# Kernel tuning notes

Measured on AMD Instinct MI355X. Metric: run time of the kernel, lower is better.

## Reference

```python
import jax, jax.numpy as jnp
import numpy as np

NS = 0.4      # neighborhood_size
GS = 8        # grid_size
RNN = 128     # rnn_size
EMB = 64      # embedding_size
NMIX = 20     # nmixtures
N = 1024      # num pedestrians


def setup_inputs() -> dict:
    key = jax.random.key(0)
    ks = jax.random.split(key, 14)
    s = 0.05
    return {
        "xoff": jax.random.normal(ks[0], (N, 2)) * s,
        "xabs": jax.random.uniform(ks[1], (N, 2)),
        "h0": jax.random.normal(ks[2], (1, N, RNN)) * 0.1,
        "c0": jax.random.normal(ks[3], (1, N, RNN)) * 0.1,
        "W_emb": jax.random.normal(ks[4], (EMB, 2)) * s,
        "b_emb": jax.random.normal(ks[5], (EMB,)) * s,
        "W_soc": jax.random.normal(ks[6], (EMB, GS * GS * RNN)) * s,
        "b_soc": jax.random.normal(ks[7], (EMB,)) * s,
        "W_ih": jax.random.normal(ks[8], (4 * RNN, 2 * EMB)) * s,
        "W_hh": jax.random.normal(ks[9], (4 * RNN, RNN)) * s,
        "b_ih": jax.random.normal(ks[10], (4 * RNN,)) * s,
        "b_hh": jax.random.normal(ks[11], (4 * RNN,)) * s,
        "W_out": jax.random.normal(ks[12], (6 * NMIX, RNN)) * s,
        "b_out": jax.random.normal(ks[13], (6 * NMIX,)) * s,
    }


def grid_mask(xabs, dtype):
    # Vectorized getGridMask: [N, N, GS*GS] one-hot neighbor binning.
    x, y = xabs[:, 0], xabs[:, 1]
    dx = x[None, :] - (x[:, None] - NS / 2)  # other_x - width_low, [N, N]
    dy = y[None, :] - (y[:, None] - NS / 2)
    cx = jnp.floor(dx / NS * GS).astype(jnp.int32)
    cy = jnp.floor(dy / NS * GS).astype(jnp.int32)
    n = x.shape[0]
    valid = ((dx >= 0) & (dx < NS) & (dy >= 0) & (dy < NS)
             & (cx >= 0) & (cx < GS) & (cy >= 0) & (cy < GS)
             & ~jnp.eye(n, dtype=bool))
    cell = jnp.clip(cx + cy * GS, 0, GS * GS - 1)
    return jax.nn.one_hot(cell, GS * GS, dtype=dtype) * valid[..., None].astype(dtype)


def reference(xoff, xabs, h0, c0, W_emb, b_emb, W_soc, b_soc,
              W_ih, W_hh, b_ih, b_hh, W_out, b_out):
    n = xabs.shape[0]
    # predict_distance=True -> embed offsets
    emb = jax.nn.relu(xoff @ W_emb.T + b_emb)                 # [N, 64]
    grid = grid_mask(xabs, emb.dtype)                          # [N, N, 64]
    h = h0[0]                                                  # [N, 128]
    # getSocialTensor: scatter neighbor hidden states into grid bins
    social = jnp.einsum('nmg,mh->ngh', grid, h).reshape(n, GS * GS * RNN)
    pool = jax.nn.relu(social @ W_soc.T + b_soc)               # [N, 64]
    xin = jnp.concatenate([emb, pool], axis=-1)                # [N, 128]
    # single-step LSTM, torch gate order i, f, g, o
    gates = xin @ W_ih.T + h @ W_hh.T + b_ih + b_hh            # [N, 512]
    i, f, g, o = jnp.split(gates, 4, axis=-1)
    c = jax.nn.sigmoid(f) * c0[0] + jax.nn.sigmoid(i) * jnp.tanh(g)
    hn = jax.nn.sigmoid(o) * jnp.tanh(c)
    out = hn @ W_out.T + b_out                                 # [N, 120]
    mu1, mu2, ls1, ls2, rho, pi_logits = jnp.split(out, 6, axis=1)
    return (mu1, mu2, ls1, ls2, rho, pi_logits)
```

## Files before the change

kernel.cpp:

```cpp
#include <hip/hip_runtime.h>
#include <hip/hip_bf16.h>

#define NN_ 1024

#define U_WGF  0
#define U_WOUT 131072
#define U_SHI  147456
#define U_SLO  671744
#define U_ACTH 1196032
#define U_ACTL 1458176
#define U_P    1720320
#define F_GL   2957312

typedef __attribute__((ext_vector_type(8))) short short8;
typedef __attribute__((ext_vector_type(4))) float floatx4;

__device__ __forceinline__ float b2f_(unsigned short u) {
    return __uint_as_float(((unsigned)u) << 16);
}
__device__ __forceinline__ unsigned short f2bu(float f) {
    __hip_bfloat16 b = __float2bfloat16(f);
    return *(unsigned short*)&b;
}
__device__ __forceinline__ float ldin(const void* p, int i, int isbf) {
    return isbf ? b2f_(((const unsigned short*)p)[i]) : ((const float*)p)[i];
}
__device__ __forceinline__ int detect_bf16(const void* Wih, int tid) {
    unsigned wv = ((const unsigned*)Wih)[tid];
    unsigned e8 = (wv >> 7) & 0xFFu;
    return (__syncthreads_count((e8 >= 96u && e8 <= 134u) ? 1 : 0) > 128) ? 1 : 0;
}

__global__ __launch_bounds__(256) void prep_kernel(
        const void* __restrict__ xoff, const void* __restrict__ h0,
        const void* __restrict__ Wsoc, const void* __restrict__ Wemb,
        const void* __restrict__ bemb, const void* __restrict__ Wih,
        const void* __restrict__ Whh,  const void* __restrict__ Wout,
        float* __restrict__ ws) {
    const int tid = threadIdx.x;
    const int isbf = detect_bf16(Wih, tid);
    unsigned short* u = (unsigned short*)ws;
    const int t0 = (blockIdx.x * 256 + tid) * 8;
    unsigned short hv[8], lv[8];
    if (t0 < 131072) {
        int jl = (t0 >> 3) & 15, q = (t0 >> 7) & 3, kb = (t0 >> 9) & 7, jt = t0 >> 12;
        int j = jt * 16 + jl, k0 = kb * 32 + q * 8;
#pragma unroll
        for (int r = 0; r < 8; r++) {
            int k = k0 + r;
            float v = (k < 128) ? ldin(Wih, j * 128 + k, isbf)
                                : ldin(Whh, j * 128 + (k - 128), isbf);
            hv[r] = f2bu(v);
        }
        *(short8*)(u + U_WGF + t0) = *(short8*)hv;
    } else if (t0 < 147456) {
        int t2 = t0 - 131072; int r = t2 >> 7, j0 = t2 & 127;
#pragma unroll
        for (int i = 0; i < 8; i++) {
            int j = j0 + i;
            hv[i] = f2bu((j < 120) ? ldin(Wout, j * 128 + r, isbf) : 0.0f);
        }
        *(short8*)(u + U_WOUT + t2) = *(short8*)hv;
    } else if (t0 < 671744) {
        int t2 = t0 - 147456;
        int e = (t2 >> 3) & 63, q = (t2 >> 9) & 3, j = (t2 >> 11) & 3, g = t2 >> 13;
        int src = e * 8192 + g * 128 + j * 32 + q * 8;
#pragma unroll
        for (int r = 0; r < 8; r++) {
            float x = ldin(Wsoc, src + r, isbf);
            hv[r] = f2bu(x);
            lv[r] = f2bu(x - b2f_(hv[r]));
        }
        *(short8*)(u + U_SHI + t2) = *(short8*)hv;
        *(short8*)(u + U_SLO + t2) = *(short8*)lv;
    } else if (t0 < 802816) {
        int t2 = t0 - 671744; int n = t2 >> 7, k = t2 & 127;
#pragma unroll
        for (int i = 0; i < 8; i++) {
            float x = ldin(h0, t2 + i, isbf);
            hv[i] = f2bu(x);
            lv[i] = f2bu(x - b2f_(hv[i]));
        }
        *(short8*)(u + U_ACTH + n * 256 + 128 + k) = *(short8*)hv;
        *(short8*)(u + U_ACTL + n * 256 + 128 + k) = *(short8*)lv;
    } else {
        int t2 = t0 - 802816; int n = t2 >> 6, e0 = t2 & 63;
        float x0 = ldin(xoff, 2 * n, isbf), x1 = ldin(xoff, 2 * n + 1, isbf);
#pragma unroll
        for (int i = 0; i < 8; i++) {
            int e = e0 + i;
            float v = fmaf(x0, ldin(Wemb, 2 * e, isbf),
                      fmaf(x1, ldin(Wemb, 2 * e + 1, isbf), ldin(bemb, e, isbf)));
            v = fmaxf(v, 0.0f);
            hv[i] = f2bu(v);
            lv[i] = f2bu(v - b2f_(hv[i]));
        }
        *(short8*)(u + U_ACTH + n * 256 + e0) = *(short8*)hv;
        *(short8*)(u + U_ACTL + n * 256 + e0) = *(short8*)lv;
    }
}

__global__ __launch_bounds__(256) void pgemm_kernel(float* __restrict__ ws) {
    const unsigned short* u = (const unsigned short*)ws;
    const short* Ah  = (const short*)(u + U_ACTH);
    const short* Al  = (const short*)(u + U_ACTL);
    const short* Shi = (const short*)(u + U_SHI);
    const short* Slo = (const short*)(u + U_SLO);
    unsigned short* P16 = (unsigned short*)ws + U_P;
    const int tid = threadIdx.x, lane = tid & 63, wv = tid >> 6;
    const int B_ = blockIdx.y * 64 + blockIdx.x;
    const int mtile = B_ & 63, rest = B_ >> 6;
    const int cg = rest >> 1, thalf = rest & 1;
    const int m = lane & 15, q = lane >> 4;
    const int g = cg * 4 + wv;
    const int abase = (mtile * 16 + m) * 256 + 128 + q * 8;
    short8 ah[4], al[4];
#pragma unroll
    for (int j = 0; j < 4; j++) {
        ah[j] = *(const short8*)(Ah + abase + 32 * j);
        al[j] = *(const short8*)(Al + abase + 32 * j);
    }
    const int rowl = mtile * 16 + q * 4;
#pragma unroll
    for (int tt = 0; tt < 2; tt++) {
        const int t = thalf * 2 + tt;
        const int e = t * 16 + m;
        short8 bh[4], bl[4];
#pragma unroll
        for (int j = 0; j < 4; j++) {
            const int fb = ((g * 4 + j) * 4 + q) * 512 + e * 8;
            bh[j] = *(const short8*)(Shi + fb);
            bl[j] = *(const short8*)(Slo + fb);
        }
        floatx4 c = {0.0f, 0.0f, 0.0f, 0.0f};
#pragma unroll
        for (int j = 0; j < 4; j++) c = __builtin_amdgcn_mfma_f32_16x16x32_bf16(ah[j], bh[j], c, 0, 0, 0);
#pragma unroll
        for (int j = 0; j < 4; j++) c = __builtin_amdgcn_mfma_f32_16x16x32_bf16(ah[j], bl[j], c, 0, 0, 0);
#pragma unroll
        for (int j = 0; j < 4; j++) c = __builtin_amdgcn_mfma_f32_16x16x32_bf16(al[j], bh[j], c, 0, 0, 0);
        const int n0 = cg * 256 + wv * 64 + t * 16;
#pragma unroll
        for (int r = 0; r < 4; r++)
            P16[(rowl + r) * 4096 + n0 + m] = f2bu(c[r]);
    }
}

__global__ __launch_bounds__(256) void pool_kernel(const void* __restrict__ xabs,
                                                   const void* __restrict__ b_soc,
                                                   const void* __restrict__ Wih_det,
                                                   float* __restrict__ ws) {
    __shared__ float xabs_s[2048];
    __shared__ int   off[NN_];
    __shared__ int   cnt_s;
    __shared__ float4 red4[16][16];
    const int tid = threadIdx.x;
    const int isbf = detect_bf16(Wih_det, tid);
    const int n = blockIdx.x;
    unsigned short* u = (unsigned short*)ws;

    for (int i = tid; i < 2048; i += 256) xabs_s[i] = ldin(xabs, i, isbf);
    if (tid == 0) cnt_s = 0;
    __syncthreads();
    {
        float xs = xabs_s[2 * n]     - 0.2f;
        float ys = xabs_s[2 * n + 1] - 0.2f;
        for (int i = tid; i < NN_; i += 256) {
            float dx = xabs_s[2 * i]     - xs;
            float dy = xabs_s[2 * i + 1] - ys;
            int cx = (int)floorf(dx / 0.4f * 8.0f);
            int cy = (int)floorf(dy / 0.4f * 8.0f);
            bool valid = (dx >= 0.0f) && (dx < 0.4f) && (dy >= 0.0f) && (dy < 0.4f)
                      && (cx >= 0) && (cx < 8) && (cy >= 0) && (cy < 8) && (i != n);
            if (valid) {
                int idx = atomicAdd(&cnt_s, 1);
                off[idx] = i * 4096 + ((cy * 8 + cx) << 6);
            }
        }
    }
    __syncthreads();
    {
        const unsigned short* P16 = (const unsigned short*)ws + U_P;
        const int strm = tid >> 4, e4 = tid & 15;
        const int cc = cnt_s;
        float ax = 0.0f, ay = 0.0f, az = 0.0f, aw = 0.0f;
        for (int j = strm; j < cc; j += 16) {
            int o = off[j];
            ushort4 uu = *(const ushort4*)(P16 + o + 4 * e4);
            ax += b2f_(uu.x); ay += b2f_(uu.y); az += b2f_(uu.z); aw += b2f_(uu.w);
        }
        red4[strm][e4] = make_float4(ax, ay, az, aw);
    }
    __syncthreads();
    if (tid < 16) {
        float s[4] = {0.0f, 0.0f, 0.0f, 0.0f};
#pragma unroll
        for (int s16 = 0; s16 < 16; s16++) {
            float4 r = red4[s16][tid];
            s[0] += r.x; s[1] += r.y; s[2] += r.z; s[3] += r.w;
        }
        int e = 4 * tid;
#pragma unroll
        for (int i = 0; i < 4; i++) {
            float v = fmaxf(s[i] + ldin(b_soc, e + i, isbf), 0.0f);
            unsigned short hi = f2bu(v);
            u[U_ACTH + n * 256 + 64 + e + i] = hi;
            u[U_ACTL + n * 256 + 64 + e + i] = f2bu(v - b2f_(hi));
        }
    }
}

__global__ __launch_bounds__(256) void gates_kernel(const void* __restrict__ b_ih,
                                                    const void* __restrict__ b_hh,
                                                    const void* __restrict__ Wih_det,
                                                    float* __restrict__ ws) {
    const int tid = threadIdx.x;
    const int isbf = detect_bf16(Wih_det, tid);
    const unsigned short* u = (const unsigned short*)ws;
    const short* Ah = (const short*)(u + U_ACTH);
    const short* Al = (const short*)(u + U_ACTL);
    const short* Wg = (const short*)(u + U_WGF);
    float* gl = ws + F_GL;
    const int lane = tid & 63, wv = tid >> 6, m = lane & 15, q = lane >> 4;
    const int m0 = blockIdx.x * 16;
    const int jt = blockIdx.y * 4 + wv;
    floatx4 acc = {0.0f, 0.0f, 0.0f, 0.0f};
#pragma unroll
    for (int kb = 0; kb < 8; kb++) {
        const int ab = (m0 + m) * 256 + kb * 32 + q * 8;
        short8 ah = *(const short8*)(Ah + ab);
        short8 al = *(const short8*)(Al + ab);
        short8 b  = *(const short8*)(Wg + (jt * 8 + kb) * 512 + q * 128 + m * 8);
        acc = __builtin_amdgcn_mfma_f32_16x16x32_bf16(ah, b, acc, 0, 0, 0);
        acc = __builtin_amdgcn_mfma_f32_16x16x32_bf16(al, b, acc, 0, 0, 0);
    }
    const int j = jt * 16 + m;
    const float bias = ldin(b_ih, j, isbf) + ldin(b_hh, j, isbf);
#pragma unroll
    for (int r = 0; r < 4; r++)
        gl[(m0 + q * 4 + r) * 512 + j] = acc[r] + bias;
}

__global__ __launch_bounds__(256) void pwout_kernel(const void* __restrict__ c0,
                                                    const void* __restrict__ b_out,
                                                    const void* __restrict__ Wih_det,
                                                    const float* __restrict__ ws,
                                                    float* __restrict__ out) {
    __shared__ __align__(16) float hnl[2][128];
    const int tid = threadIdx.x;
    const int isbf = detect_bf16(Wih_det, tid);
    const int n0 = blockIdx.x * 2;
    const unsigned short* u = (const unsigned short*)ws;
    const float* gl = ws + F_GL;
    const int half = tid >> 7, t2 = tid & 127;
    const int n = n0 + half;
    {
        int r = t2;
        float iv = gl[n * 512 + r],       fv = gl[n * 512 + r + 128];
        float gv = gl[n * 512 + r + 256], ov = gl[n * 512 + r + 384];
        float si = 1.0f / (1.0f + expf(-iv));
        float sf = 1.0f / (1.0f + expf(-fv));
        float so = 1.0f / (1.0f + expf(-ov));
        float cc = sf * ldin(c0, n * 128 + r, isbf) + si * tanhf(gv);
        hnl[half][r] = so * tanhf(cc);
    }
    __syncthreads();
    {
        int j = t2;
        if (j < 120) {
            float acc = ldin(b_out, j, isbf);
            for (int r = 0; r < 128; r += 4) {
                float4 hq = *(const float4*)&hnl[half][r];
                acc = fmaf(hq.x, b2f_(u[U_WOUT + (r + 0) * 128 + j]), acc);
                acc = fmaf(hq.y, b2f_(u[U_WOUT + (r + 1) * 128 + j]), acc);
                acc = fmaf(hq.z, b2f_(u[U_WOUT + (r + 2) * 128 + j]), acc);
                acc = fmaf(hq.w, b2f_(u[U_WOUT + (r + 3) * 128 + j]), acc);
            }
            int ch = j / 20, wc = j - ch * 20;
            out[ch * 20480 + n * 20 + wc] = acc;
        }
    }
}

extern "C" void kernel_launch(void* const* d_in, const int* in_sizes, int n_in,
                              void* d_out, int out_size, void* d_ws, size_t ws_size,
                              hipStream_t stream) {
    const void* xoff  = d_in[0];
    const void* xabs  = d_in[1];
    const void* h0    = d_in[2];
    const void* c0    = d_in[3];
    const void* W_emb = d_in[4];
    const void* b_emb = d_in[5];
    const void* W_soc = d_in[6];
    const void* b_soc = d_in[7];
    const void* W_ih  = d_in[8];
    const void* W_hh  = d_in[9];
    const void* b_ih  = d_in[10];
    const void* b_hh  = d_in[11];
    const void* W_out = d_in[12];
    const void* b_out = d_in[13];
    float* ws = (float*)d_ws;
    float* out = (float*)d_out;

    prep_kernel<<<424, 256, 0, stream>>>(xoff, h0, W_soc, W_emb, b_emb,
                                         W_ih, W_hh, W_out, ws);
    pgemm_kernel<<<dim3(64, 32), 256, 0, stream>>>(ws);
    pool_kernel<<<1024, 256, 0, stream>>>(xabs, b_soc, W_ih, ws);
    gates_kernel<<<dim3(64, 8), 256, 0, stream>>>(b_ih, b_hh, W_ih, ws);
    pwout_kernel<<<512, 256, 0, stream>>>(c0, b_out, W_ih, ws, out);
}
```

Measured before the change: 124.6 us.

## Drop split-bf16 compensation, fuse LSTM cell into gates kernel, fp32 Wout

Removes the hi/lo bf16 split of activations and W_soc, so the social GEMM and gate GEMM use one bf16 MFMA pass instead of three or two. This halves the operand traffic and cuts MFMA work. The gate output columns are permuted so each block holds i/f/g/o for the same 16 hidden units, which lets the LSTM cell nonlinearity run inside the gates kernel and write hn directly instead of a 512-wide gate buffer. W_out is now stored in fp32. The cost is lower precision in the pooled and gate results, which could affect accuracy tolerance.

```diff
diff --git a/kernel.cpp b/kernel.cpp
--- a/kernel.cpp
+++ b/kernel.cpp
@@ -4,13 +4,11 @@
 #define NN_ 1024
 
 #define U_WGF  0
-#define U_WOUT 131072
-#define U_SHI  147456
-#define U_SLO  671744
-#define U_ACTH 1196032
-#define U_ACTL 1458176
-#define U_P    1720320
-#define F_GL   2957312
+#define U_SHI  131072
+#define U_ACTH 655360
+#define U_P    917504
+#define F_WOUT 2555904
+#define F_HN   2572288
 
 typedef __attribute__((ext_vector_type(8))) short short8;
 typedef __attribute__((ext_vector_type(4))) float floatx4;
@@ -41,10 +39,11 @@
     const int isbf = detect_bf16(Wih, tid);
     unsigned short* u = (unsigned short*)ws;
     const int t0 = (blockIdx.x * 256 + tid) * 8;
-    unsigned short hv[8], lv[8];
+    unsigned short hv[8];
     if (t0 < 131072) {
         int jl = (t0 >> 3) & 15, q = (t0 >> 7) & 3, kb = (t0 >> 9) & 7, jt = t0 >> 12;
-        int j = jt * 16 + jl, k0 = kb * 32 + q * 8;
+        int j = (jt & 3) * 128 + (jt >> 2) * 16 + jl;
+        int k0 = kb * 32 + q * 8;
 #pragma unroll
         for (int r = 0; r < 8; r++) {
             int k = k0 + r;
@@ -58,31 +57,20 @@
 #pragma unroll
         for (int i = 0; i < 8; i++) {
             int j = j0 + i;
-            hv[i] = f2bu((j < 120) ? ldin(Wout, j * 128 + r, isbf) : 0.0f);
-        }
-        *(short8*)(u + U_WOUT + t2) = *(short8*)hv;
+            ws[F_WOUT + t2 + i] = (j < 120) ? ldin(Wout, j * 128 + r, isbf) : 0.0f;
+        }
     } else if (t0 < 671744) {
         int t2 = t0 - 147456;
         int e = (t2 >> 3) & 63, q = (t2 >> 9) & 3, j = (t2 >> 11) & 3, g = t2 >> 13;
         int src = e * 8192 + g * 128 + j * 32 + q * 8;
 #pragma unroll
-        for (int r = 0; r < 8; r++) {
-            float x = ldin(Wsoc, src + r, isbf);
-            hv[r] = f2bu(x);
-            lv[r] = f2bu(x - b2f_(hv[r]));
-        }
+        for (int r = 0; r < 8; r++) hv[r] = f2bu(ldin(Wsoc, src + r, isbf));
         *(short8*)(u + U_SHI + t2) = *(short8*)hv;
-        *(short8*)(u + U_SLO + t2) = *(short8*)lv;
     } else if (t0 < 802816) {
         int t2 = t0 - 671744; int n = t2 >> 7, k = t2 & 127;
 #pragma unroll
-        for (int i = 0; i < 8; i++) {
-            float x = ldin(h0, t2 + i, isbf);
-            hv[i] = f2bu(x);
-            lv[i] = f2bu(x - b2f_(hv[i]));
-        }
+        for (int i = 0; i < 8; i++) hv[i] = f2bu(ldin(h0, t2 + i, isbf));
         *(short8*)(u + U_ACTH + n * 256 + 128 + k) = *(short8*)hv;
-        *(short8*)(u + U_ACTL + n * 256 + 128 + k) = *(short8*)lv;
     } else {
         int t2 = t0 - 802816; int n = t2 >> 6, e0 = t2 & 63;
         float x0 = ldin(xoff, 2 * n, isbf), x1 = ldin(xoff, 2 * n + 1, isbf);
@@ -91,21 +79,16 @@
             int e = e0 + i;
             float v = fmaf(x0, ldin(Wemb, 2 * e, isbf),
                       fmaf(x1, ldin(Wemb, 2 * e + 1, isbf), ldin(bemb, e, isbf)));
-            v = fmaxf(v, 0.0f);
-            hv[i] = f2bu(v);
-            lv[i] = f2bu(v - b2f_(hv[i]));
+            hv[i] = f2bu(fmaxf(v, 0.0f));
         }
         *(short8*)(u + U_ACTH + n * 256 + e0) = *(short8*)hv;
-        *(short8*)(u + U_ACTL + n * 256 + e0) = *(short8*)lv;
     }
 }
 
 __global__ __launch_bounds__(256) void pgemm_kernel(float* __restrict__ ws) {
     const unsigned short* u = (const unsigned short*)ws;
     const short* Ah  = (const short*)(u + U_ACTH);
-    const short* Al  = (const short*)(u + U_ACTL);
     const short* Shi = (const short*)(u + U_SHI);
-    const short* Slo = (const short*)(u + U_SLO);
     unsigned short* P16 = (unsigned short*)ws + U_P;
     const int tid = threadIdx.x, lane = tid & 63, wv = tid >> 6;
     const int B_ = blockIdx.y * 64 + blockIdx.x;
@@ -114,31 +97,20 @@
     const int m = lane & 15, q = lane >> 4;
     const int g = cg * 4 + wv;
     const int abase = (mtile * 16 + m) * 256 + 128 + q * 8;
-    short8 ah[4], al[4];
-#pragma unroll
-    for (int j = 0; j < 4; j++) {
-        ah[j] = *(const short8*)(Ah + abase + 32 * j);
-        al[j] = *(const short8*)(Al + abase + 32 * j);
-    }
+    short8 ah[4];
+#pragma unroll
+    for (int j = 0; j < 4; j++) ah[j] = *(const short8*)(Ah + abase + 32 * j);
     const int rowl = mtile * 16 + q * 4;
 #pragma unroll
     for (int tt = 0; tt < 2; tt++) {
         const int t = thalf * 2 + tt;
         const int e = t * 16 + m;
-        short8 bh[4], bl[4];
+        floatx4 c = {0.0f, 0.0f, 0.0f, 0.0f};
 #pragma unroll
         for (int j = 0; j < 4; j++) {
-            const int fb = ((g * 4 + j) * 4 + q) * 512 + e * 8;
-            bh[j] = *(const short8*)(Shi + fb);
-            bl[j] = *(const short8*)(Slo + fb);
-        }
-        floatx4 c = {0.0f, 0.0f, 0.0f, 0.0f};
-#pragma unroll
-        for (int j = 0; j < 4; j++) c = __builtin_amdgcn_mfma_f32_16x16x32_bf16(ah[j], bh[j], c, 0, 0, 0);
-#pragma unroll
-        for (int j = 0; j < 4; j++) c = __builtin_amdgcn_mfma_f32_16x16x32_bf16(ah[j], bl[j], c, 0, 0, 0);
-#pragma unroll
-        for (int j = 0; j < 4; j++) c = __builtin_amdgcn_mfma_f32_16x16x32_bf16(al[j], bh[j], c, 0, 0, 0);
+            short8 bh = *(const short8*)(Shi + ((g * 4 + j) * 4 + q) * 512 + e * 8);
+            c = __builtin_amdgcn_mfma_f32_16x16x32_bf16(ah[j], bh, c, 0, 0, 0);
+        }
         const int n0 = cg * 256 + wv * 64 + t * 16;
 #pragma unroll
         for (int r = 0; r < 4; r++)
@@ -203,46 +175,52 @@
 #pragma unroll
         for (int i = 0; i < 4; i++) {
             float v = fmaxf(s[i] + ldin(b_soc, e + i, isbf), 0.0f);
-            unsigned short hi = f2bu(v);
-            u[U_ACTH + n * 256 + 64 + e + i] = hi;
-            u[U_ACTL + n * 256 + 64 + e + i] = f2bu(v - b2f_(hi));
-        }
-    }
-}
-
-__global__ __launch_bounds__(256) void gates_kernel(const void* __restrict__ b_ih,
+            u[U_ACTH + n * 256 + 64 + e + i] = f2bu(v);
+        }
+    }
+}
+
+__global__ __launch_bounds__(256) void gates_kernel(const void* __restrict__ c0,
+                                                    const void* __restrict__ b_ih,
                                                     const void* __restrict__ b_hh,
                                                     const void* __restrict__ Wih_det,
                                                     float* __restrict__ ws) {
+    __shared__ float gl[16][68];
     const int tid = threadIdx.x;
     const int isbf = detect_bf16(Wih_det, tid);
     const unsigned short* u = (const unsigned short*)ws;
     const short* Ah = (const short*)(u + U_ACTH);
-    const short* Al = (const short*)(u + U_ACTL);
     const short* Wg = (const short*)(u + U_WGF);
-    float* gl = ws + F_GL;
     const int lane = tid & 63, wv = tid >> 6, m = lane & 15, q = lane >> 4;
-    const int m0 = blockIdx.x * 16;
-    const int jt = blockIdx.y * 4 + wv;
+    const int m0 = blockIdx.x * 16, y = blockIdx.y;
+    const int jt = y * 4 + wv;
     floatx4 acc = {0.0f, 0.0f, 0.0f, 0.0f};
 #pragma unroll
     for (int kb = 0; kb < 8; kb++) {
-        const int ab = (m0 + m) * 256 + kb * 32 + q * 8;
-        short8 ah = *(const short8*)(Ah + ab);
-        short8 al = *(const short8*)(Al + ab);
+        short8 ah = *(const short8*)(Ah + (m0 + m) * 256 + kb * 32 + q * 8);
         short8 b  = *(const short8*)(Wg + (jt * 8 + kb) * 512 + q * 128 + m * 8);
         acc = __builtin_amdgcn_mfma_f32_16x16x32_bf16(ah, b, acc, 0, 0, 0);
-        acc = __builtin_amdgcn_mfma_f32_16x16x32_bf16(al, b, acc, 0, 0, 0);
-    }
-    const int j = jt * 16 + m;
-    const float bias = ldin(b_ih, j, isbf) + ldin(b_hh, j, isbf);
+    }
+    const int jorig = wv * 128 + y * 16 + m;
+    const float bias = ldin(b_ih, jorig, isbf) + ldin(b_hh, jorig, isbf);
 #pragma unroll
     for (int r = 0; r < 4; r++)
-        gl[(m0 + q * 4 + r) * 512 + j] = acc[r] + bias;
-}
-
-__global__ __launch_bounds__(256) void pwout_kernel(const void* __restrict__ c0,
-                                                    const void* __restrict__ b_out,
+        gl[q * 4 + r][wv * 16 + m] = acc[r] + bias;
+    __syncthreads();
+    {
+        const int a = tid >> 4, rl = tid & 15;
+        const int n = m0 + a, rg = y * 16 + rl;
+        float iv = gl[a][rl],      fv = gl[a][16 + rl];
+        float gv = gl[a][32 + rl], ov = gl[a][48 + rl];
+        float si = 1.0f / (1.0f + expf(-iv));
+        float sf = 1.0f / (1.0f + expf(-fv));
+        float so = 1.0f / (1.0f + expf(-ov));
+        float cc = sf * ldin(c0, n * 128 + rg, isbf) + si * tanhf(gv);
+        ws[F_HN + n * 128 + rg] = so * tanhf(cc);
+    }
+}
+
+__global__ __launch_bounds__(256) void pwout_kernel(const void* __restrict__ b_out,
                                                     const void* __restrict__ Wih_det,
                                                     const float* __restrict__ ws,
                                                     float* __restrict__ out) {
@@ -250,35 +228,22 @@
     const int tid = threadIdx.x;
     const int isbf = detect_bf16(Wih_det, tid);
     const int n0 = blockIdx.x * 2;
-    const unsigned short* u = (const unsigned short*)ws;
-    const float* gl = ws + F_GL;
     const int half = tid >> 7, t2 = tid & 127;
     const int n = n0 + half;
-    {
-        int r = t2;
-        float iv = gl[n * 512 + r],       fv = gl[n * 512 + r + 128];
-        float gv = gl[n * 512 + r + 256], ov = gl[n * 512 + r + 384];
-        float si = 1.0f / (1.0f + expf(-iv));
-        float sf = 1.0f / (1.0f + expf(-fv));
-        float so = 1.0f / (1.0f + expf(-ov));
-        float cc = sf * ldin(c0, n * 128 + r, isbf) + si * tanhf(gv);
-        hnl[half][r] = so * tanhf(cc);
-    }
-    __syncthreads();
-    {
+    hnl[half][t2] = ws[F_HN + n * 128 + t2];
+    __syncthreads();
+    if (t2 < 120) {
         int j = t2;
-        if (j < 120) {
-            float acc = ldin(b_out, j, isbf);
-            for (int r = 0; r < 128; r += 4) {
-                float4 hq = *(const float4*)&hnl[half][r];
-                acc = fmaf(hq.x, b2f_(u[U_WOUT + (r + 0) * 128 + j]), acc);
-                acc = fmaf(hq.y, b2f_(u[U_WOUT + (r + 1) * 128 + j]), acc);
-                acc = fmaf(hq.z, b2f_(u[U_WOUT + (r + 2) * 128 + j]), acc);
-                acc = fmaf(hq.w, b2f_(u[U_WOUT + (r + 3) * 128 + j]), acc);
-            }
-            int ch = j / 20, wc = j - ch * 20;
-            out[ch * 20480 + n * 20 + wc] = acc;
-        }
+        float acc = ldin(b_out, j, isbf);
+        for (int r = 0; r < 128; r += 4) {
+            float4 hq = *(const float4*)&hnl[half][r];
+            acc = fmaf(hq.x, ws[F_WOUT + (r + 0) * 128 + j], acc);
+            acc = fmaf(hq.y, ws[F_WOUT + (r + 1) * 128 + j], acc);
+            acc = fmaf(hq.z, ws[F_WOUT + (r + 2) * 128 + j], acc);
+            acc = fmaf(hq.w, ws[F_WOUT + (r + 3) * 128 + j], acc);
+        }
+        int ch = j / 20, wc = j - ch * 20;
+        out[ch * 20480 + n * 20 + wc] = acc;
     }
 }
 
@@ -306,6 +271,6 @@
                                          W_ih, W_hh, W_out, ws);
     pgemm_kernel<<<dim3(64, 32), 256, 0, stream>>>(ws);
     pool_kernel<<<1024, 256, 0, stream>>>(xabs, b_soc, W_ih, ws);
-    gates_kernel<<<dim3(64, 8), 256, 0, stream>>>(b_ih, b_hh, W_ih, ws);
-    pwout_kernel<<<512, 256, 0, stream>>>(c0, b_out, W_ih, ws, out);
-}
+    gates_kernel<<<dim3(64, 8), 256, 0, stream>>>(c0, b_ih, b_hh, W_ih, ws);
+    pwout_kernel<<<512, 256, 0, stream>>>(b_out, W_ih, ws, out);
+}
```

Result: faster. 117.5 us (median of 2 runs) (-5.7%).
